# Kernel tuning notes

Measured on AMD Instinct MI355X. Metric: run time of the kernel, lower is better.

The kernel has to match this reference:

```python
import jax, jax.numpy as jnp
import numpy as np

B, U, V = 4, 64, 256
IN_DIM, STATE_DIM, CODE_DIM = 768, 768, 384
NUM_HEADS, HEAD_DIM = 8, 64
INNER = NUM_HEADS * HEAD_DIM  # 512
SCALE = HEAD_DIM ** 0.5


def _ln(x, g, b, eps=1e-5):
    mu = jnp.mean(x, axis=-1, keepdims=True)
    var = jnp.var(x, axis=-1, keepdims=True)
    return (x - mu) * jax.lax.rsqrt(var + eps) * g + b


def setup_inputs() -> dict:
    key = jax.random.key(0)
    ks = jax.random.split(key, 12)
    def w(k, shape, s=0.02):
        return jax.random.normal(k, shape, jnp.float32) * s
    return {
        "receiver_states": jax.random.normal(ks[0], (B, U, STATE_DIM), jnp.float32),
        "receiver_codes": jax.random.normal(ks[1], (B, U, CODE_DIM), jnp.float32),
        "sender_states": jax.random.normal(ks[2], (B, V, IN_DIM), jnp.float32),
        "ln_r_g": jnp.ones((STATE_DIM,), jnp.float32),
        "ln_r_b": jnp.zeros((STATE_DIM,), jnp.float32),
        "ln_s_g": jnp.ones((IN_DIM,), jnp.float32),
        "ln_s_b": jnp.zeros((IN_DIM,), jnp.float32),
        "Wq": w(ks[3], (STATE_DIM, INNER)), "bq": jnp.zeros((INNER,), jnp.float32), "Wmq": w(ks[4], (CODE_DIM, STATE_DIM)),
        "Wk": w(ks[5], (IN_DIM, INNER)),   "bk": jnp.zeros((INNER,), jnp.float32), "Wmk": w(ks[6], (CODE_DIM, IN_DIM)),
        "Wv": w(ks[7], (IN_DIM, INNER)),   "bv": jnp.zeros((INNER,), jnp.float32), "Wmv": w(ks[8], (CODE_DIM, IN_DIM)),
        "We": w(ks[9], (INNER, STATE_DIM)), "be": jnp.zeros((STATE_DIM,), jnp.float32), "Wme": w(ks[10], (CODE_DIM, INNER)),
        "gamma": jnp.ones((STATE_DIM,), jnp.float32),  # LayerScale, init 1.0
    }


def reference(receiver_states, receiver_codes, sender_states,
              ln_r_g, ln_r_b, ln_s_g, ln_s_b,
              Wq, bq, Wmq, Wk, bk, Wmk, Wv, bv, Wmv, We, be, Wme, gamma):
    r = _ln(receiver_states, ln_r_g, ln_r_b)   # (b,u,ds)
    s = _ln(sender_states, ln_s_g, ln_s_b)     # (b,v,di)
    # ModFC: y = (x * (1 + ctx @ Wm)) @ W + b  (code-conditioned input modulation)
    q = (r * (1.0 + receiver_codes @ Wmq)) @ Wq + bq          # (b,u,inner)
    mk = 1.0 + receiver_codes @ Wmk                           # (b,u,di)
    mv = 1.0 + receiver_codes @ Wmv                           # (b,u,di)
    xs = s[:, :, None, :]                                     # (b,v,1,di)
    k = (xs * mk[:, None, :, :]) @ Wk + bk                    # (b,v,u,inner)
    v = (xs * mv[:, None, :, :]) @ Wv + bv                    # (b,v,u,inner)
    qh = q.reshape(B, U, NUM_HEADS, HEAD_DIM)
    kh = k.reshape(B, V, U, NUM_HEADS, HEAD_DIM)
    vh = v.reshape(B, V, U, NUM_HEADS, HEAD_DIM)
    scores = jnp.einsum('buhc,bvuhc->bhuv', qh, kh) / SCALE   # (b,h,u,v)
    weights = jax.nn.softmax(scores, axis=-1)
    msg = jnp.einsum('bhuv,bvuhc->buhc', weights, vh).reshape(B, U, INNER)
    out = (msg * (1.0 + receiver_codes @ Wme)) @ We + be      # exit ModFC -> (b,u,ds)
    out = out * gamma                                         # LayerScale
    return receiver_states + out                              # residual
```

## Files before the change

kernel.cpp:

```cpp
#include <hip/hip_runtime.h>


#define DD 768
#define CDIM 384
#define NH 8
#define HD 64
#define INNER 512
#define VV 256

__device__ __forceinline__ void fma4(float4& a, float s, const float4& b) {
  a.x += s * b.x; a.y += s * b.y; a.z += s * b.z; a.w += s * b.w;
}

template <int K, int NS>
__device__ __forceinline__ void gcore(const float* __restrict__ A0, int lda,
                                      const float* __restrict__ Bp,
                                      float4& a0, float4& a1, float4& a2,
                                      float4& a3) {
  float4 b0[8], b1[8];
#pragma unroll
  for (int i = 0; i < 8; i++) b0[i] = *(const float4*)(Bp + (size_t)i * NS);
  const float* Bq = Bp + (size_t)8 * NS;
#pragma unroll 1
  for (int kk = 0; kk < K; kk += 16) {
#pragma unroll
    for (int i = 0; i < 8; i++) b1[i] = *(const float4*)(Bq + (size_t)i * NS);
    Bq += (size_t)8 * NS;
#pragma unroll
    for (int i = 0; i < 8; i++) {
      float4 bv = b0[i]; int k = kk + i;
      fma4(a0, A0[k], bv); fma4(a1, A0[lda + k], bv);
      fma4(a2, A0[2 * lda + k], bv); fma4(a3, A0[3 * lda + k], bv);
    }
    if (kk + 16 < K) {
#pragma unroll
      for (int i = 0; i < 8; i++) b0[i] = *(const float4*)(Bq + (size_t)i * NS);
      Bq += (size_t)8 * NS;
    }
#pragma unroll
    for (int i = 0; i < 8; i++) {
      float4 bv = b1[i]; int k = kk + 8 + i;
      fma4(a0, A0[k], bv); fma4(a1, A0[lda + k], bv);
      fma4(a2, A0[2 * lda + k], bv); fma4(a3, A0[3 * lda + k], bv);
    }
  }
}

__global__ __launch_bounds__(256, 2) void k_s1(
    const float* __restrict__ ss, const float* __restrict__ rs,
    const float* __restrict__ g_s, const float* __restrict__ b_s,
    const float* __restrict__ g_r, const float* __restrict__ b_r,
    const float* __restrict__ codes, const float* __restrict__ Wmq,
    const float* __restrict__ Wmk, const float* __restrict__ Wmv,
    const float* __restrict__ Wme, const float* __restrict__ Wk,
    float* __restrict__ s_ln, float* __restrict__ r_ln,
    float* __restrict__ cp, float* __restrict__ WkT) {
  __shared__ float SB[6144];
  int bid = blockIdx.x, t = threadIdx.x;
  if (bid < 176) {
    int nc = bid % 11, mb = bid / 11;
    int base = nc * 256;
    const float* W; int N, colW;
    if (base < 768)       { W = Wmq; N = DD;    colW = base; }
    else if (base < 1536) { W = Wmk; N = DD;    colW = base - 768; }
    else if (base < 2304) { W = Wmv; N = DD;    colW = base - 1536; }
    else                  { W = Wme; N = INNER; colW = base - 2304; }
    int m0 = mb * 16;
#pragma unroll
    for (int p = 0; p < 24; p++) {
      int idx = p * 256 + t, r = idx / 384, k = idx % 384;
      SB[idx] = codes[(size_t)(m0 + r) * CDIM + k];
    }
    __syncthreads();
    int kl = t & 63, wid = t >> 6;
    const float* A0 = SB + (wid * 4) * 384;
    float4 a0 = {0,0,0,0}, a1 = {0,0,0,0}, a2 = {0,0,0,0}, a3 = {0,0,0,0};
    if (N == DD)
      gcore<384, DD>(A0, 384, W + colW + 4 * kl, a0, a1, a2, a3);
    else
      gcore<384, INNER>(A0, 384, W + colW + 4 * kl, a0, a1, a2, a3);
    int m = m0 + wid * 4, gcol = base + 4 * kl;
    *(float4*)(cp + (size_t)m * 2816 + gcol) = a0;
    *(float4*)(cp + (size_t)(m + 1) * 2816 + gcol) = a1;
    *(float4*)(cp + (size_t)(m + 2) * 2816 + gcol) = a2;
    *(float4*)(cp + (size_t)(m + 3) * 2816 + gcol) = a3;
  } else if (bid < 272) {
    int tid = bid - 176;
    int d0 = (tid >> 3) * 64, c0 = (tid & 7) * 64;
    int j = t & 63, i0 = t >> 6;
#pragma unroll
    for (int p = 0; p < 16; p++) {
      int i = p * 4 + i0;
      SB[i * 65 + j] = Wk[(size_t)(d0 + i) * INNER + c0 + j];
    }
    __syncthreads();
#pragma unroll
    for (int p = 0; p < 16; p++) {
      int i = p * 4 + i0;
      WkT[(size_t)(c0 + i) * DD + d0 + j] = SB[j * 65 + i];
    }
  } else {
    int rr = bid - 272;
    const float *x, *g, *bb; float* y; int r;
    if (rr < 1024) { x = ss; g = g_s; bb = b_s; y = s_ln; r = rr; }
    else           { x = rs; g = g_r; bb = b_r; y = r_ln; r = rr - 1024; }
    const float* xr = x + (size_t)r * DD;
    float v0 = xr[t], v1 = xr[t + 256], v2 = xr[t + 512];
    float s = v0 + v1 + v2, sq = v0 * v0 + v1 * v1 + v2 * v2;
    for (int o = 32; o > 0; o >>= 1) {
      s += __shfl_down(s, o, 64); sq += __shfl_down(sq, o, 64);
    }
    int wid = t >> 6, lane = t & 63;
    if (lane == 0) { SB[wid] = s; SB[wid + 4] = sq; }
    __syncthreads();
    float sum = SB[0] + SB[1] + SB[2] + SB[3];
    float ssq = SB[4] + SB[5] + SB[6] + SB[7];
    float mu = sum * (1.0f / 768.0f);
    float var = ssq * (1.0f / 768.0f) - mu * mu;
    float rstd = rsqrtf(var + 1e-5f);
    float* yr = y + (size_t)r * DD;
    yr[t]       = (v0 - mu) * rstd * g[t]       + bb[t];
    yr[t + 256] = (v1 - mu) * rstd * g[t + 256] + bb[t + 256];
    yr[t + 512] = (v2 - mu) * rstd * g[t + 512] + bb[t + 512];
  }
}

__global__ __launch_bounds__(256, 2) void k_s2(
    const float* __restrict__ s_ln, const float* __restrict__ r_ln,
    const float* __restrict__ cp, const float* __restrict__ Wq,
    float* __restrict__ sT, float* __restrict__ qp) {
  __shared__ float SB[4160];
  int bid = blockIdx.x, t = threadIdx.x;
  if (bid < 128) {
    int ks = bid & 3, tile = bid >> 2, nc = tile & 1, mb = tile >> 1;
    int m0 = mb * 16, col0 = nc * 256, k0 = ks * 192;
#pragma unroll
    for (int p = 0; p < 12; p++) {
      int idx = p * 256 + t, r = idx / 192, k = idx % 192;
      int d = k0 + k;
      float mqv = cp[(size_t)(m0 + r) * 2816 + d] + 1.0f;
      SB[idx] = r_ln[(size_t)(m0 + r) * DD + d] * mqv;
    }
    __syncthreads();
    int kl = t & 63, wid = t >> 6;
    int col = col0 + 4 * kl;
    const float* A0 = SB + (wid * 4) * 192;
    float4 a0 = {0,0,0,0}, a1 = {0,0,0,0}, a2 = {0,0,0,0}, a3 = {0,0,0,0};
    gcore<192, INNER>(A0, 192, Wq + (size_t)k0 * INNER + col, a0, a1, a2, a3);
    int m = m0 + wid * 4;
    float* dst = qp + (size_t)ks * (256 * INNER);
    *(float4*)(dst + (size_t)m * INNER + col) = a0;
    *(float4*)(dst + (size_t)(m + 1) * INNER + col) = a1;
    *(float4*)(dst + (size_t)(m + 2) * INNER + col) = a2;
    *(float4*)(dst + (size_t)(m + 3) * INNER + col) = a3;
  } else {
    int tid = bid - 128;
    int vt = tid & 3, dt = (tid >> 2) % 12, b = tid / 48;
    int v0 = vt * 64, d0 = dt * 64;
    int j = t & 63, i0 = t >> 6;
#pragma unroll
    for (int p = 0; p < 16; p++) {
      int i = p * 4 + i0;
      SB[i * 65 + j] = s_ln[(size_t)(b * VV + v0 + i) * DD + d0 + j];
    }
    __syncthreads();
#pragma unroll
    for (int p = 0; p < 16; p++) {
      int i = p * 4 + i0;
      sT[((size_t)b * DD + d0 + i) * VV + v0 + j] = SB[j * 65 + i];
    }
  }
}

__global__ __launch_bounds__(256, 2) void k_s3(
    const float* __restrict__ qp, const float* __restrict__ bq,
    const float* __restrict__ WkT, const float* __restrict__ cp,
    const float* __restrict__ bk, float* __restrict__ qm,
    float* __restrict__ qbk) {
  __shared__ float SB[1024];
  int bid = blockIdx.x, t = threadIdx.x;
  if (bid < 384) {
    int h = bid & 7, dc = (bid >> 3) % 3, mb = bid / 24;
    int m0 = mb * 16;
#pragma unroll
    for (int p = 0; p < 4; p++) {
      int idx = p * 256 + t, r = idx >> 6, c = idx & 63;
      int i = h * HD + c;
      size_t off = (size_t)(m0 + r) * INNER + i;
      SB[idx] = qp[off] + qp[131072 + off] + qp[262144 + off] +
                qp[393216 + off] + bq[i];
    }
    __syncthreads();
    int kl = t & 63, wid = t >> 6;
    int col = dc * 256 + 4 * kl;
    const float* A0 = SB + (wid * 4) * HD;
    float4 a0 = {0,0,0,0}, a1 = {0,0,0,0}, a2 = {0,0,0,0}, a3 = {0,0,0,0};
    gcore<64, DD>(A0, HD, WkT + (size_t)(h * HD) * DD + col, a0, a1, a2, a3);
#pragma unroll
    for (int j = 0; j < 4; j++) {
      float4 a = (j == 0) ? a0 : (j == 1) ? a1 : (j == 2) ? a2 : a3;
      int m = m0 + wid * 4 + j;
      const float* mkp = cp + (size_t)m * 2816 + 768 + col;
      float4 o = {a.x * (mkp[0] + 1.0f), a.y * (mkp[1] + 1.0f),
                  a.z * (mkp[2] + 1.0f), a.w * (mkp[3] + 1.0f)};
      *(float4*)(qm + ((size_t)m * NH + h) * DD + col) = o;
    }
  } else {
    int m = bid - 384;
    size_t off = (size_t)m * INNER;
    SB[t] = (qp[off + t] + qp[131072 + off + t] + qp[262144 + off + t] +
             qp[393216 + off + t] + bq[t]) * bk[t];
    int t2 = t + 256;
    SB[t2] = (qp[off + t2] + qp[131072 + off + t2] + qp[262144 + off + t2] +
              qp[393216 + off + t2] + bq[t2]) * bk[t2];
    __syncthreads();
    if (t < 8) {
      float a = 0.f;
      for (int c = 0; c < HD; c++) a += SB[t * HD + c];
      qbk[m * NH + t] = a;
    }
  }
}

__global__ __launch_bounds__(256, 2) void k_s4(
    const float* __restrict__ qm, const float* __restrict__ sT,
    float* __restrict__ scp) {
  __shared__ float SB[3072];
  int bid = blockIdx.x, t = threadIdx.x;
  int ks = bid & 3, b = (bid >> 2) & 3, mb = bid >> 4;
  int gi0 = b * 512 + mb * 16, k0 = ks * 192;
#pragma unroll
  for (int p = 0; p < 12; p++) {
    int idx = p * 256 + t, r = idx / 192, k = idx % 192;
    SB[idx] = qm[(size_t)(gi0 + r) * DD + k0 + k];
  }
  __syncthreads();
  int kl = t & 63, wid = t >> 6;
  int col = 4 * kl;
  const float* A0 = SB + (wid * 4) * 192;
  float4 a0 = {0,0,0,0}, a1 = {0,0,0,0}, a2 = {0,0,0,0}, a3 = {0,0,0,0};
  gcore<192, VV>(A0, 192, sT + ((size_t)b * DD + k0) * VV + col, a0, a1, a2, a3);
  int gi = gi0 + wid * 4;
  float* dst = scp + (size_t)ks * (2048 * VV);
  *(float4*)(dst + (size_t)gi * VV + col) = a0;
  *(float4*)(dst + (size_t)(gi + 1) * VV + col) = a1;
  *(float4*)(dst + (size_t)(gi + 2) * VV + col) = a2;
  *(float4*)(dst + (size_t)(gi + 3) * VV + col) = a3;
}

__global__ __launch_bounds__(256, 2) void k_s5(
    const float* __restrict__ scp, const float* __restrict__ qbk,
    const float* __restrict__ s_ln, const float* __restrict__ cp,
    float* __restrict__ wsm) {
  __shared__ float SC[4096];
  int bid = blockIdx.x, t = threadIdx.x;
  int dc = bid % 3, up = (bid / 3) % 32, b = bid / 96;
  int gi0 = b * 512 + up * 16;
#pragma unroll
  for (int p = 0; p < 16; p++) {
    int idx = p * 256 + t, r = idx >> 8, c = idx & 255;
    size_t o = (size_t)(gi0 + r) * VV + c;
    float v = scp[o] + scp[524288 + o] + scp[1048576 + o] + scp[1572864 + o];
    int m = b * 64 + up * 2 + (r >> 3), h = r & 7;
    SC[idx] = (v + qbk[m * NH + h]) * 0.125f;
  }
  __syncthreads();
  int wid = t >> 6, lane = t & 63;
#pragma unroll
  for (int j = 0; j < 4; j++) {
    int r = wid * 4 + j;
    float x0 = SC[r * 256 + lane],       x1 = SC[r * 256 + lane + 64];
    float x2 = SC[r * 256 + lane + 128], x3 = SC[r * 256 + lane + 192];
    float mx = fmaxf(fmaxf(x0, x1), fmaxf(x2, x3));
    for (int o = 1; o < 64; o <<= 1) mx = fmaxf(mx, __shfl_xor(mx, o, 64));
    float e0 = __expf(x0 - mx), e1 = __expf(x1 - mx);
    float e2 = __expf(x2 - mx), e3 = __expf(x3 - mx);
    float sm = e0 + e1 + e2 + e3;
    for (int o = 1; o < 64; o <<= 1) sm += __shfl_xor(sm, o, 64);
    float rinv = 1.0f / sm;
    SC[r * 256 + lane] = e0 * rinv;       SC[r * 256 + lane + 64] = e1 * rinv;
    SC[r * 256 + lane + 128] = e2 * rinv; SC[r * 256 + lane + 192] = e3 * rinv;
  }
  __syncthreads();
  int kl = t & 63;
  int col = dc * 256 + 4 * kl;
  const float* A0 = SC + (wid * 4) * 256;
  float4 a0 = {0,0,0,0}, a1 = {0,0,0,0}, a2 = {0,0,0,0}, a3 = {0,0,0,0};
  gcore<VV, DD>(A0, 256, s_ln + (size_t)(b * VV) * DD + col, a0, a1, a2, a3);
#pragma unroll
  for (int j = 0; j < 4; j++) {
    float4 a = (j == 0) ? a0 : (j == 1) ? a1 : (j == 2) ? a2 : a3;
    int r = wid * 4 + j;
    int ul = r >> 3, h = r & 7, m = b * 64 + up * 2 + ul;
    const float* mvp = cp + (size_t)m * 2816 + 1536 + col;
    float4 o = {a.x * (mvp[0] + 1.0f), a.y * (mvp[1] + 1.0f),
                a.z * (mvp[2] + 1.0f), a.w * (mvp[3] + 1.0f)};
    *(float4*)(wsm + ((size_t)h * 256 + m) * DD + col) = o;
  }
}

__global__ __launch_bounds__(256, 2) void k_s6(
    const float* __restrict__ wsm, const float* __restrict__ Wv,
    float* __restrict__ mmp) {
  __shared__ float AL[6144];
  int bid = blockIdx.x, t = threadIdx.x;
  int hp = bid & 1, ks = (bid >> 1) & 7, mb = bid >> 4;
  int h0 = hp * 4, m0 = mb * 16, k0 = ks * 96;
#pragma unroll
  for (int p = 0; p < 24; p++) {
    int idx = p * 256 + t;
    int e = idx / 1536, rem = idx % 1536, r = rem / 96, k = rem % 96;
    AL[idx] = wsm[((size_t)(h0 + e) * 256 + m0 + r) * DD + k0 + k];
  }
  __syncthreads();
  int kl = t & 63, wid = t >> 6;
  int hs = kl >> 4, c4 = 4 * (kl & 15);
  int colg = h0 * HD + hs * HD + c4;
  const float* A0 = AL + (hs * 16 + wid * 4) * 96;
  float4 a0 = {0,0,0,0}, a1 = {0,0,0,0}, a2 = {0,0,0,0}, a3 = {0,0,0,0};
  gcore<96, INNER>(A0, 96, Wv + (size_t)k0 * INNER + colg, a0, a1, a2, a3);
  float* dst = mmp + (size_t)ks * (256 * INNER);
  int m = m0 + wid * 4;
  *(float4*)(dst + (size_t)m * INNER + colg) = a0;
  *(float4*)(dst + (size_t)(m + 1) * INNER + colg) = a1;
  *(float4*)(dst + (size_t)(m + 2) * INNER + colg) = a2;
  *(float4*)(dst + (size_t)(m + 3) * INNER + colg) = a3;
}

__global__ __launch_bounds__(256, 2) void k_s7(
    const float* __restrict__ mmp, const float* __restrict__ bvv,
    const float* __restrict__ cp, const float* __restrict__ We,
    float* __restrict__ op) {
  __shared__ float AL[1024];
  int bid = blockIdx.x, t = threadIdx.x;
  int ks = bid & 7, dc = (bid >> 3) % 3, mb = bid / 24;
  int m0 = mb * 16, k0 = ks * 64;
#pragma unroll
  for (int p = 0; p < 4; p++) {
    int idx = p * 256 + t, r = idx >> 6, k = idx & 63;
    int i = k0 + k;
    size_t off = (size_t)(m0 + r) * INNER + i;
    float v = mmp[off] + mmp[131072 + off] + mmp[262144 + off] +
              mmp[393216 + off] + mmp[524288 + off] + mmp[655360 + off] +
              mmp[786432 + off] + mmp[917504 + off];
    float mev = cp[(size_t)(m0 + r) * 2816 + 2304 + i] + 1.0f;
    AL[idx] = (v + bvv[i]) * mev;
  }
  __syncthreads();
  int kl = t & 63, wid = t >> 6;
  int col = dc * 256 + 4 * kl;
  const float* A0 = AL + (wid * 4) * 64;
  float4 a0 = {0,0,0,0}, a1 = {0,0,0,0}, a2 = {0,0,0,0}, a3 = {0,0,0,0};
  gcore<64, DD>(A0, 64, We + (size_t)k0 * DD + col, a0, a1, a2, a3);
  float* dst = op + (size_t)ks * (256 * DD);
  int m = m0 + wid * 4;
  *(float4*)(dst + (size_t)m * DD + col) = a0;
  *(float4*)(dst + (size_t)(m + 1) * DD + col) = a1;
  *(float4*)(dst + (size_t)(m + 2) * DD + col) = a2;
  *(float4*)(dst + (size_t)(m + 3) * DD + col) = a3;
}

__global__ __launch_bounds__(256) void k_s8(
    const float* __restrict__ op, const float* __restrict__ be,
    const float* __restrict__ gamma, const float* __restrict__ rs,
    float* __restrict__ outp) {
  int m = blockIdx.x, t = threadIdx.x;
#pragma unroll
  for (int j = 0; j < 3; j++) {
    int d = t + j * 256;
    size_t off = (size_t)m * DD + d;
    float v = op[off] + op[196608 + off] + op[393216 + off] +
              op[589824 + off] + op[786432 + off] + op[983040 + off] +
              op[1179648 + off] + op[1376256 + off];
    outp[off] = rs[off] + (v + be[d]) * gamma[d];
  }
}

extern "C" void kernel_launch(void* const* d_in, const int* in_sizes, int n_in,
                              void* d_out, int out_size, void* d_ws, size_t ws_size,
                              hipStream_t stream) {
  const float* rs     = (const float*)d_in[0];
  const float* codes  = (const float*)d_in[1];
  const float* ss     = (const float*)d_in[2];
  const float* ln_r_g = (const float*)d_in[3];
  const float* ln_r_b = (const float*)d_in[4];
  const float* ln_s_g = (const float*)d_in[5];
  const float* ln_s_b = (const float*)d_in[6];
  const float* Wq  = (const float*)d_in[7];
  const float* bq  = (const float*)d_in[8];
  const float* Wk  = (const float*)d_in[10];
  const float* bk  = (const float*)d_in[11];
  const float* Wmq = (const float*)d_in[9];
  const float* Wmk = (const float*)d_in[12];
  const float* Wv  = (const float*)d_in[13];
  const float* bv  = (const float*)d_in[14];
  const float* Wmv = (const float*)d_in[15];
  const float* We  = (const float*)d_in[16];
  const float* be  = (const float*)d_in[17];
  const float* Wme = (const float*)d_in[18];
  const float* gamma = (const float*)d_in[19];

  float* w = (float*)d_ws;
  float* s_ln = w;
  float* r_ln = w + 786432;
  float* WkT  = w + 983040;
  float* qp   = w + 1376256;
  float* sT   = w + 1900544;
  float* cp   = w + 2686976;
  float* qbk  = w + 3407872;
  float* qm   = w + 3409920;
  float* scp  = w + 4982784;
  float* wsm  = qm;
  float* mmp  = r_ln;
  float* op   = scp;

  k_s1<<<dim3(1552), 256, 0, stream>>>(ss, rs, ln_s_g, ln_s_b, ln_r_g, ln_r_b,
                                       codes, Wmq, Wmk, Wmv, Wme, Wk,
                                       s_ln, r_ln, cp, WkT);
  k_s2<<<dim3(320), 256, 0, stream>>>(s_ln, r_ln, cp, Wq, sT, qp);
  k_s3<<<dim3(640), 256, 0, stream>>>(qp, bq, WkT, cp, bk, qm, qbk);
  k_s4<<<dim3(512), 256, 0, stream>>>(qm, sT, scp);
  k_s5<<<dim3(384), 256, 0, stream>>>(scp, qbk, s_ln, cp, wsm);
  k_s6<<<dim3(256), 256, 0, stream>>>(wsm, Wv, mmp);
  k_s7<<<dim3(384), 256, 0, stream>>>(mmp, bv, cp, We, op);
  k_s8<<<dim3(256), 256, 0, stream>>>(op, be, gamma, rs, (float*)d_out);
}
```

Measured before the change: 198.2 us.

## Fuse final split-K reduction into atomics and vectorize shared A-operand reads

The output is pre-initialized in the layernorm stage with residual plus be*gamma. The exit GEMM then atomically adds its gamma-scaled split-K partials straight into the output, which removes the partial buffer and the separate reduction kernel. The GEMM core now reads the shared-memory A operand as float4 instead of scalar loads, cutting LDS instruction count. The k_s6 shared layout is padded so its float4 reads stay aligned. Float atomics make the summation order nondeterministic and add atomic traffic on the output.

```diff
diff --git a/kernel.cpp b/kernel.cpp
--- a/kernel.cpp
+++ b/kernel.cpp
@@ -27,10 +27,17 @@
     for (int i = 0; i < 8; i++) b1[i] = *(const float4*)(Bq + (size_t)i * NS);
     Bq += (size_t)8 * NS;
 #pragma unroll
-    for (int i = 0; i < 8; i++) {
-      float4 bv = b0[i]; int k = kk + i;
-      fma4(a0, A0[k], bv); fma4(a1, A0[lda + k], bv);
-      fma4(a2, A0[2 * lda + k], bv); fma4(a3, A0[3 * lda + k], bv);
+    for (int c = 0; c < 2; c++) {
+      int kb = kk + c * 4;
+      float4 f0 = *(const float4*)(A0 + kb);
+      float4 f1 = *(const float4*)(A0 + lda + kb);
+      float4 f2 = *(const float4*)(A0 + 2 * lda + kb);
+      float4 f3 = *(const float4*)(A0 + 3 * lda + kb);
+      float4 bv;
+      bv = b0[c*4+0]; fma4(a0,f0.x,bv); fma4(a1,f1.x,bv); fma4(a2,f2.x,bv); fma4(a3,f3.x,bv);
+      bv = b0[c*4+1]; fma4(a0,f0.y,bv); fma4(a1,f1.y,bv); fma4(a2,f2.y,bv); fma4(a3,f3.y,bv);
+      bv = b0[c*4+2]; fma4(a0,f0.z,bv); fma4(a1,f1.z,bv); fma4(a2,f2.z,bv); fma4(a3,f3.z,bv);
+      bv = b0[c*4+3]; fma4(a0,f0.w,bv); fma4(a1,f1.w,bv); fma4(a2,f2.w,bv); fma4(a3,f3.w,bv);
     }
     if (kk + 16 < K) {
 #pragma unroll
@@ -38,10 +45,17 @@
       Bq += (size_t)8 * NS;
     }
 #pragma unroll
-    for (int i = 0; i < 8; i++) {
-      float4 bv = b1[i]; int k = kk + 8 + i;
-      fma4(a0, A0[k], bv); fma4(a1, A0[lda + k], bv);
-      fma4(a2, A0[2 * lda + k], bv); fma4(a3, A0[3 * lda + k], bv);
+    for (int c = 0; c < 2; c++) {
+      int kb = kk + 8 + c * 4;
+      float4 f0 = *(const float4*)(A0 + kb);
+      float4 f1 = *(const float4*)(A0 + lda + kb);
+      float4 f2 = *(const float4*)(A0 + 2 * lda + kb);
+      float4 f3 = *(const float4*)(A0 + 3 * lda + kb);
+      float4 bv;
+      bv = b1[c*4+0]; fma4(a0,f0.x,bv); fma4(a1,f1.x,bv); fma4(a2,f2.x,bv); fma4(a3,f3.x,bv);
+      bv = b1[c*4+1]; fma4(a0,f0.y,bv); fma4(a1,f1.y,bv); fma4(a2,f2.y,bv); fma4(a3,f3.y,bv);
+      bv = b1[c*4+2]; fma4(a0,f0.z,bv); fma4(a1,f1.z,bv); fma4(a2,f2.z,bv); fma4(a3,f3.z,bv);
+      bv = b1[c*4+3]; fma4(a0,f0.w,bv); fma4(a1,f1.w,bv); fma4(a2,f2.w,bv); fma4(a3,f3.w,bv);
     }
   }
 }
@@ -53,9 +67,11 @@
     const float* __restrict__ codes, const float* __restrict__ Wmq,
     const float* __restrict__ Wmk, const float* __restrict__ Wmv,
     const float* __restrict__ Wme, const float* __restrict__ Wk,
+    const float* __restrict__ be, const float* __restrict__ gamma,
     float* __restrict__ s_ln, float* __restrict__ r_ln,
-    float* __restrict__ cp, float* __restrict__ WkT) {
-  __shared__ float SB[6144];
+    float* __restrict__ cp, float* __restrict__ WkT,
+    float* __restrict__ outp) {
+  __shared__ __align__(16) float SB[6400];
   int bid = blockIdx.x, t = threadIdx.x;
   if (bid < 176) {
     int nc = bid % 11, mb = bid / 11;
@@ -101,9 +117,9 @@
     }
   } else {
     int rr = bid - 272;
-    const float *x, *g, *bb; float* y; int r;
-    if (rr < 1024) { x = ss; g = g_s; bb = b_s; y = s_ln; r = rr; }
-    else           { x = rs; g = g_r; bb = b_r; y = r_ln; r = rr - 1024; }
+    const float *x, *g, *bb; float* y; int r; bool isR;
+    if (rr < 1024) { x = ss; g = g_s; bb = b_s; y = s_ln; r = rr; isR = false; }
+    else           { x = rs; g = g_r; bb = b_r; y = r_ln; r = rr - 1024; isR = true; }
     const float* xr = x + (size_t)r * DD;
     float v0 = xr[t], v1 = xr[t + 256], v2 = xr[t + 512];
     float s = v0 + v1 + v2, sq = v0 * v0 + v1 * v1 + v2 * v2;
@@ -122,6 +138,12 @@
     yr[t]       = (v0 - mu) * rstd * g[t]       + bb[t];
     yr[t + 256] = (v1 - mu) * rstd * g[t + 256] + bb[t + 256];
     yr[t + 512] = (v2 - mu) * rstd * g[t + 512] + bb[t + 512];
+    if (isR) {
+      float* orow = outp + (size_t)r * DD;
+      orow[t]       = v0 + be[t]       * gamma[t];
+      orow[t + 256] = v1 + be[t + 256] * gamma[t + 256];
+      orow[t + 512] = v2 + be[t + 512] * gamma[t + 512];
+    }
   }
 }
 
@@ -129,10 +151,10 @@
     const float* __restrict__ s_ln, const float* __restrict__ r_ln,
     const float* __restrict__ cp, const float* __restrict__ Wq,
     float* __restrict__ sT, float* __restrict__ qp) {
-  __shared__ float SB[4160];
+  __shared__ __align__(16) float SB[4160];
   int bid = blockIdx.x, t = threadIdx.x;
   if (bid < 128) {
-    int ks = bid & 3, tile = bid >> 2, nc = tile & 1, mb = tile >> 1;
+    int ks = bid & 3, t2 = bid >> 2, nc = t2 & 1, mb = t2 >> 1;
     int m0 = mb * 16, col0 = nc * 256, k0 = ks * 192;
 #pragma unroll
     for (int p = 0; p < 12; p++) {
@@ -177,7 +199,7 @@
     const float* __restrict__ WkT, const float* __restrict__ cp,
     const float* __restrict__ bk, float* __restrict__ qm,
     float* __restrict__ qbk) {
-  __shared__ float SB[1024];
+  __shared__ __align__(16) float SB[1024];
   int bid = blockIdx.x, t = threadIdx.x;
   if (bid < 384) {
     int h = bid & 7, dc = (bid >> 3) % 3, mb = bid / 24;
@@ -225,7 +247,7 @@
 __global__ __launch_bounds__(256, 2) void k_s4(
     const float* __restrict__ qm, const float* __restrict__ sT,
     float* __restrict__ scp) {
-  __shared__ float SB[3072];
+  __shared__ __align__(16) float SB[3072];
   int bid = blockIdx.x, t = threadIdx.x;
   int ks = bid & 3, b = (bid >> 2) & 3, mb = bid >> 4;
   int gi0 = b * 512 + mb * 16, k0 = ks * 192;
@@ -252,7 +274,7 @@
     const float* __restrict__ scp, const float* __restrict__ qbk,
     const float* __restrict__ s_ln, const float* __restrict__ cp,
     float* __restrict__ wsm) {
-  __shared__ float SC[4096];
+  __shared__ __align__(16) float SB[4096];
   int bid = blockIdx.x, t = threadIdx.x;
   int dc = bid % 3, up = (bid / 3) % 32, b = bid / 96;
   int gi0 = b * 512 + up * 16;
@@ -262,15 +284,15 @@
     size_t o = (size_t)(gi0 + r) * VV + c;
     float v = scp[o] + scp[524288 + o] + scp[1048576 + o] + scp[1572864 + o];
     int m = b * 64 + up * 2 + (r >> 3), h = r & 7;
-    SC[idx] = (v + qbk[m * NH + h]) * 0.125f;
+    SB[idx] = (v + qbk[m * NH + h]) * 0.125f;
   }
   __syncthreads();
   int wid = t >> 6, lane = t & 63;
 #pragma unroll
   for (int j = 0; j < 4; j++) {
     int r = wid * 4 + j;
-    float x0 = SC[r * 256 + lane],       x1 = SC[r * 256 + lane + 64];
-    float x2 = SC[r * 256 + lane + 128], x3 = SC[r * 256 + lane + 192];
+    float x0 = SB[r * 256 + lane],       x1 = SB[r * 256 + lane + 64];
+    float x2 = SB[r * 256 + lane + 128], x3 = SB[r * 256 + lane + 192];
     float mx = fmaxf(fmaxf(x0, x1), fmaxf(x2, x3));
     for (int o = 1; o < 64; o <<= 1) mx = fmaxf(mx, __shfl_xor(mx, o, 64));
     float e0 = __expf(x0 - mx), e1 = __expf(x1 - mx);
@@ -278,13 +300,13 @@
     float sm = e0 + e1 + e2 + e3;
     for (int o = 1; o < 64; o <<= 1) sm += __shfl_xor(sm, o, 64);
     float rinv = 1.0f / sm;
-    SC[r * 256 + lane] = e0 * rinv;       SC[r * 256 + lane + 64] = e1 * rinv;
-    SC[r * 256 + lane + 128] = e2 * rinv; SC[r * 256 + lane + 192] = e3 * rinv;
+    SB[r * 256 + lane] = e0 * rinv;       SB[r * 256 + lane + 64] = e1 * rinv;
+    SB[r * 256 + lane + 128] = e2 * rinv; SB[r * 256 + lane + 192] = e3 * rinv;
   }
   __syncthreads();
   int kl = t & 63;
   int col = dc * 256 + 4 * kl;
-  const float* A0 = SC + (wid * 4) * 256;
+  const float* A0 = SB + (wid * 4) * 256;
   float4 a0 = {0,0,0,0}, a1 = {0,0,0,0}, a2 = {0,0,0,0}, a3 = {0,0,0,0};
   gcore<VV, DD>(A0, 256, s_ln + (size_t)(b * VV) * DD + col, a0, a1, a2, a3);
 #pragma unroll
@@ -302,7 +324,7 @@
 __global__ __launch_bounds__(256, 2) void k_s6(
     const float* __restrict__ wsm, const float* __restrict__ Wv,
     float* __restrict__ mmp) {
-  __shared__ float AL[6144];
+  __shared__ __align__(16) float SB[6400];
   int bid = blockIdx.x, t = threadIdx.x;
   int hp = bid & 1, ks = (bid >> 1) & 7, mb = bid >> 4;
   int h0 = hp * 4, m0 = mb * 16, k0 = ks * 96;
@@ -310,13 +332,14 @@
   for (int p = 0; p < 24; p++) {
     int idx = p * 256 + t;
     int e = idx / 1536, rem = idx % 1536, r = rem / 96, k = rem % 96;
-    AL[idx] = wsm[((size_t)(h0 + e) * 256 + m0 + r) * DD + k0 + k];
+    SB[e * 1540 + r * 96 + k] =
+        wsm[((size_t)(h0 + e) * 256 + m0 + r) * DD + k0 + k];
   }
   __syncthreads();
   int kl = t & 63, wid = t >> 6;
   int hs = kl >> 4, c4 = 4 * (kl & 15);
   int colg = h0 * HD + hs * HD + c4;
-  const float* A0 = AL + (hs * 16 + wid * 4) * 96;
+  const float* A0 = SB + hs * 1540 + (wid * 4) * 96;
   float4 a0 = {0,0,0,0}, a1 = {0,0,0,0}, a2 = {0,0,0,0}, a3 = {0,0,0,0};
   gcore<96, INNER>(A0, 96, Wv + (size_t)k0 * INNER + colg, a0, a1, a2, a3);
   float* dst = mmp + (size_t)ks * (256 * INNER);
@@ -330,8 +353,8 @@
 __global__ __launch_bounds__(256, 2) void k_s7(
     const float* __restrict__ mmp, const float* __restrict__ bvv,
     const float* __restrict__ cp, const float* __restrict__ We,
-    float* __restrict__ op) {
-  __shared__ float AL[1024];
+    const float* __restrict__ gamma, float* __restrict__ outp) {
+  __shared__ __align__(16) float SB[1024];
   int bid = blockIdx.x, t = threadIdx.x;
   int ks = bid & 7, dc = (bid >> 3) % 3, mb = bid / 24;
   int m0 = mb * 16, k0 = ks * 64;
@@ -344,35 +367,24 @@
               mmp[393216 + off] + mmp[524288 + off] + mmp[655360 + off] +
               mmp[786432 + off] + mmp[917504 + off];
     float mev = cp[(size_t)(m0 + r) * 2816 + 2304 + i] + 1.0f;
-    AL[idx] = (v + bvv[i]) * mev;
+    SB[idx] = (v + bvv[i]) * mev;
   }
   __syncthreads();
   int kl = t & 63, wid = t >> 6;
   int col = dc * 256 + 4 * kl;
-  const float* A0 = AL + (wid * 4) * 64;
+  const float* A0 = SB + (wid * 4) * 64;
   float4 a0 = {0,0,0,0}, a1 = {0,0,0,0}, a2 = {0,0,0,0}, a3 = {0,0,0,0};
   gcore<64, DD>(A0, 64, We + (size_t)k0 * DD + col, a0, a1, a2, a3);
-  float* dst = op + (size_t)ks * (256 * DD);
+  float4 g4 = *(const float4*)(gamma + col);
   int m = m0 + wid * 4;
-  *(float4*)(dst + (size_t)m * DD + col) = a0;
-  *(float4*)(dst + (size_t)(m + 1) * DD + col) = a1;
-  *(float4*)(dst + (size_t)(m + 2) * DD + col) = a2;
-  *(float4*)(dst + (size_t)(m + 3) * DD + col) = a3;
-}
-
-__global__ __launch_bounds__(256) void k_s8(
-    const float* __restrict__ op, const float* __restrict__ be,
-    const float* __restrict__ gamma, const float* __restrict__ rs,
-    float* __restrict__ outp) {
-  int m = blockIdx.x, t = threadIdx.x;
-#pragma unroll
-  for (int j = 0; j < 3; j++) {
-    int d = t + j * 256;
-    size_t off = (size_t)m * DD + d;
-    float v = op[off] + op[196608 + off] + op[393216 + off] +
-              op[589824 + off] + op[786432 + off] + op[983040 + off] +
-              op[1179648 + off] + op[1376256 + off];
-    outp[off] = rs[off] + (v + be[d]) * gamma[d];
+#pragma unroll
+  for (int j = 0; j < 4; j++) {
+    float4 a = (j == 0) ? a0 : (j == 1) ? a1 : (j == 2) ? a2 : a3;
+    float* orow = outp + (size_t)(m + j) * DD + col;
+    unsafeAtomicAdd(orow + 0, a.x * g4.x);
+    unsafeAtomicAdd(orow + 1, a.y * g4.y);
+    unsafeAtomicAdd(orow + 2, a.z * g4.z);
+    unsafeAtomicAdd(orow + 3, a.w * g4.w);
   }
 }
 
@@ -388,9 +400,9 @@
   const float* ln_s_b = (const float*)d_in[6];
   const float* Wq  = (const float*)d_in[7];
   const float* bq  = (const float*)d_in[8];
+  const float* Wmq = (const float*)d_in[9];
   const float* Wk  = (const float*)d_in[10];
   const float* bk  = (const float*)d_in[11];
-  const float* Wmq = (const float*)d_in[9];
   const float* Wmk = (const float*)d_in[12];
   const float* Wv  = (const float*)d_in[13];
   const float* bv  = (const float*)d_in[14];
@@ -412,16 +424,14 @@
   float* scp  = w + 4982784;
   float* wsm  = qm;
   float* mmp  = r_ln;
-  float* op   = scp;
 
   k_s1<<<dim3(1552), 256, 0, stream>>>(ss, rs, ln_s_g, ln_s_b, ln_r_g, ln_r_b,
-                                       codes, Wmq, Wmk, Wmv, Wme, Wk,
-                                       s_ln, r_ln, cp, WkT);
+                                       codes, Wmq, Wmk, Wmv, Wme, Wk, be, gamma,
+                                       s_ln, r_ln, cp, WkT, (float*)d_out);
   k_s2<<<dim3(320), 256, 0, stream>>>(s_ln, r_ln, cp, Wq, sT, qp);
   k_s3<<<dim3(640), 256, 0, stream>>>(qp, bq, WkT, cp, bk, qm, qbk);
   k_s4<<<dim3(512), 256, 0, stream>>>(qm, sT, scp);
   k_s5<<<dim3(384), 256, 0, stream>>>(scp, qbk, s_ln, cp, wsm);
   k_s6<<<dim3(256), 256, 0, stream>>>(wsm, Wv, mmp);
-  k_s7<<<dim3(384), 256, 0, stream>>>(mmp, bv, cp, We, op);
-  k_s8<<<dim3(256), 256, 0, stream>>>(op, be, gamma, rs, (float*)d_out);
-}
+  k_s7<<<dim3(384), 256, 0, stream>>>(mmp, bv, cp, We, gamma, (float*)d_out);
+}
```

Result: slower. 213.3 us (+7.7%).
